# Optimization experiments

Measured on AMD Instinct MI355X. Metric: run time of the kernel, lower is better.

The kernel has to match this reference:

```python
import jax, jax.numpy as jnp
import numpy as np

B, N, D = 16, 2048, 64

def setup_inputs() -> dict:
    key = jax.random.key(0)
    kq, kk, kv = jax.random.split(key, 3)
    q = jax.random.normal(kq, (B, N, D), dtype=jnp.float32)
    k = jax.random.normal(kk, (B, N, D), dtype=jnp.float32)
    v = jax.random.normal(kv, (B, N, D), dtype=jnp.float32)
    scale = jnp.float32(1.0 / np.sqrt(D))  # canonical 1/sqrt(d_head)
    return {"q": q, "k": k, "v": v, "scale": scale}

def reference(q, k, v, scale):
    # attention = softmax((q @ k^T) * scale) over key axis; dropout p=0.0 is identity
    scores = jnp.einsum('bqd,bkd->bqk', q, k) * scale  # [B,N,N]
    attention = jax.nn.softmax(scores, axis=2)
    context = jnp.einsum('bqk,bkd->bqd', attention, v)  # [B,N,D]
    return (context, attention)
```

## Files before the change

### kernel.cpp

```cpp
#include <hip/hip_runtime.h>

#define Bb 16
#define Nn 2048
#define Dd 64

typedef __attribute__((ext_vector_type(8))) short s16x8;
typedef __attribute__((ext_vector_type(4))) float fx4;

__device__ __forceinline__ unsigned short f2bf(float f) {
  union { float f; unsigned u; } v; v.f = f;
  unsigned r = v.u + 0x7FFFu + ((v.u >> 16) & 1u);
  return (unsigned short)(r >> 16);
}

__global__ void k_cvtK(const float* __restrict__ K, unsigned short* __restrict__ Kb) {
  int i = blockIdx.x * 256 + threadIdx.x;
  float4 f = ((const float4*)K)[i];
  ushort4 o;
  o.x = f2bf(f.x); o.y = f2bf(f.y); o.z = f2bf(f.z); o.w = f2bf(f.w);
  ((ushort4*)Kb)[i] = o;
}

__global__ void k_transV(const float* __restrict__ V, unsigned short* __restrict__ VT) {
  __shared__ float tile[32][33];
  int b = blockIdx.z;
  int j0 = blockIdx.x * 32, d0 = blockIdx.y * 32;
  int tx = threadIdx.x, ty = threadIdx.y;
  const float* Vb = V + (size_t)b * Nn * Dd;
  unsigned short* Tb = VT + (size_t)b * Dd * Nn;
  for (int r = ty; r < 32; r += 8)
    tile[r][tx] = Vb[(size_t)(j0 + r) * Dd + d0 + tx];
  __syncthreads();
  for (int r = ty; r < 32; r += 8)
    Tb[(size_t)(d0 + r) * Nn + j0 + tx] = f2bf(tile[tx][r]);
}

__global__ __launch_bounds__(256) void k_attn(
    const float* __restrict__ Q, const unsigned short* __restrict__ Kbf,
    const unsigned short* __restrict__ VTbf, const float* __restrict__ scale_p,
    float* __restrict__ ctx, float* __restrict__ att) {
  const int id = blockIdx.x;
  const int swz = ((id & 7) << 8) | (id >> 3);
  const int b = swz >> 7;
  const int q0 = (swz & 127) << 4;

  const int tid = threadIdx.x;
  const int wave = tid >> 6, lane = tid & 63;
  const int nl = lane & 15, quad = lane >> 4;
  const int qrow = q0 + nl;
  const float c2 = scale_p[0] * 1.44269504088896341f;

  __shared__ float sm[4][16];
  __shared__ float sl[4][16];
  __shared__ __align__(16) float obf[4 * 1024];
  char* pbw = (char*)obf + wave * 4096;

  s16x8 qb[2];
  {
    const float* qp = Q + ((size_t)b * Nn + qrow) * Dd + quad * 8;
#pragma unroll
    for (int kt = 0; kt < 2; ++kt) {
      float4 f0 = *(const float4*)(qp + kt * 32);
      float4 f1 = *(const float4*)(qp + kt * 32 + 4);
      s16x8 t;
      t[0] = (short)f2bf(f0.x); t[1] = (short)f2bf(f0.y);
      t[2] = (short)f2bf(f0.z); t[3] = (short)f2bf(f0.w);
      t[4] = (short)f2bf(f1.x); t[5] = (short)f2bf(f1.y);
      t[6] = (short)f2bf(f1.z); t[7] = (short)f2bf(f1.w);
      qb[kt] = t;
    }
  }
  const unsigned short* Kb = Kbf + (size_t)b * Nn * Dd;
  const unsigned short* VTb = VTbf + (size_t)b * Dd * Nn;
  float* attb = att + (size_t)b * Nn * Nn;

  float m = -3.0e38f, l = 0.0f;

  for (int t = 0; t < 4; ++t) {
    const int k0 = (wave * 4 + t) * 128;
    fx4 s[8];
#pragma unroll
    for (int nt = 0; nt < 8; ++nt) s[nt] = (fx4){0.f, 0.f, 0.f, 0.f};
#pragma unroll
    for (int nt = 0; nt < 8; ++nt) {
      const s16x8* ka =
          (const s16x8*)(Kb + ((size_t)(k0 + nt * 16 + nl)) * Dd + quad * 8);
      s[nt] = __builtin_amdgcn_mfma_f32_16x16x32_bf16(ka[0], qb[0], s[nt], 0, 0, 0);
      s[nt] = __builtin_amdgcn_mfma_f32_16x16x32_bf16(ka[4], qb[1], s[nt], 0, 0, 0);
    }
    float x0 = s[0][0], x1 = s[0][1], x2 = s[0][2], x3 = s[0][3];
#pragma unroll
    for (int nt = 1; nt < 8; ++nt) {
      x0 = fmaxf(x0, s[nt][0]); x1 = fmaxf(x1, s[nt][1]);
      x2 = fmaxf(x2, s[nt][2]); x3 = fmaxf(x3, s[nt][3]);
    }
    float lm = fmaxf(fmaxf(x0, x1), fmaxf(x2, x3));
    float mn = fmaxf(m, lm * c2);
    float a0 = 0.f, a1 = 0.f, a2 = 0.f, a3 = 0.f;
#pragma unroll
    for (int nt = 0; nt < 8; ++nt) {
      a0 += exp2f(fmaf(s[nt][0], c2, -mn));
      a1 += exp2f(fmaf(s[nt][1], c2, -mn));
      a2 += exp2f(fmaf(s[nt][2], c2, -mn));
      a3 += exp2f(fmaf(s[nt][3], c2, -mn));
    }
    float ls = (a0 + a1) + (a2 + a3);
    l = l * exp2f(m - mn) + ls;
    m = mn;
  }
#pragma unroll
  for (int mask = 16; mask <= 32; mask <<= 1) {
    float om = __shfl_xor(m, mask, 64);
    float ol = __shfl_xor(l, mask, 64);
    float mn = fmaxf(m, om);
    l = l * exp2f(m - mn) + ol * exp2f(om - mn);
    m = mn;
  }
  if (lane < 16) { sm[wave][lane] = m; sl[wave][lane] = l; }
  __syncthreads();
  float rinv;
  {
    float M = sm[0][nl], L = sl[0][nl];
#pragma unroll
    for (int j = 1; j < 4; ++j) {
      float mj = sm[j][nl], lj = sl[j][nl];
      float mn = fmaxf(M, mj);
      L = L * exp2f(M - mn) + lj * exp2f(mj - mn);
      M = mn;
    }
    m = M;
    rinv = 1.0f / L;
  }

  fx4 o[4];
#pragma unroll
  for (int d = 0; d < 4; ++d) o[d] = (fx4){0.f, 0.f, 0.f, 0.f};

  for (int t = 0; t < 4; ++t) {
    const int k0 = (wave * 4 + t) * 128;
    fx4 s[8];
#pragma unroll
    for (int nt = 0; nt < 8; ++nt) s[nt] = (fx4){0.f, 0.f, 0.f, 0.f};
#pragma unroll
    for (int nt = 0; nt < 8; ++nt) {
      const s16x8* ka =
          (const s16x8*)(Kb + ((size_t)(k0 + nt * 16 + nl)) * Dd + quad * 8);
      s[nt] = __builtin_amdgcn_mfma_f32_16x16x32_bf16(ka[0], qb[0], s[nt], 0, 0, 0);
      s[nt] = __builtin_amdgcn_mfma_f32_16x16x32_bf16(ka[4], qb[1], s[nt], 0, 0, 0);
    }
#pragma unroll
    for (int nt = 0; nt < 8; ++nt) {
#pragma unroll
      for (int r = 0; r < 4; ++r)
        s[nt][r] = exp2f(fmaf(s[nt][r], c2, -m)) * rinv;
      unsigned long long pk =
          (unsigned long long)f2bf(s[nt][0]) |
          ((unsigned long long)f2bf(s[nt][1]) << 16) |
          ((unsigned long long)f2bf(s[nt][2]) << 32) |
          ((unsigned long long)f2bf(s[nt][3]) << 48);
      *(unsigned long long*)(pbw + nl * 256 +
                             ((nt * 32 + quad * 8) ^ ((nl & 7) << 4))) = pk;
    }
#pragma unroll
    for (int kt = 0; kt < 4; ++kt) {
      s16x8 pa = *(const s16x8*)(pbw + nl * 256 +
                                 ((kt * 64 + quad * 16) ^ ((nl & 7) << 4)));
#pragma unroll
      for (int ntd = 0; ntd < 4; ++ntd) {
        s16x8 vb = *(const s16x8*)(VTb + ((size_t)(ntd * 16 + nl)) * Nn + k0 +
                                   kt * 32 + quad * 8);
        o[ntd] = __builtin_amdgcn_mfma_f32_16x16x32_bf16(pa, vb, o[ntd], 0, 0, 0);
      }
    }
    __builtin_amdgcn_sched_barrier(0);
#pragma unroll
    for (int nt = 0; nt < 8; ++nt)
      __builtin_nontemporal_store(
          s[nt], (fx4*)(attb + (size_t)qrow * Nn + k0 + nt * 16 + quad * 4));
  }

  {
    float* myob = obf + wave * 1024;
#pragma unroll
    for (int ntd = 0; ntd < 4; ++ntd)
#pragma unroll
      for (int r = 0; r < 4; ++r) {
        const int row = quad * 4 + r;
        const int unit = ntd * 4 + (nl >> 2);
        const int su = unit ^ (row & 7);
        myob[row * 64 + su * 4 + (nl & 3)] = o[ntd][r];
      }
  }
  __syncthreads();
  {
    const int row = tid >> 4;
    const int un = tid & 15;
    const int su = un ^ (row & 7);
    fx4 a = *(const fx4*)&obf[row * 64 + su * 4];
#pragma unroll
    for (int j = 1; j < 4; ++j) {
      fx4 tt = *(const fx4*)&obf[j * 1024 + row * 64 + su * 4];
      a[0] += tt[0]; a[1] += tt[1]; a[2] += tt[2]; a[3] += tt[3];
    }
    *(fx4*)(ctx + ((size_t)b * Nn + q0 + row) * Dd + un * 4) = a;
  }
}

extern "C" void kernel_launch(void* const* d_in, const int* in_sizes, int n_in,
                              void* d_out, int out_size, void* d_ws, size_t ws_size,
                              hipStream_t stream) {
  const float* q = (const float*)d_in[0];
  const float* k = (const float*)d_in[1];
  const float* v = (const float*)d_in[2];
  const float* scale = (const float*)d_in[3];

  float* ctx = (float*)d_out;
  float* att = ctx + (size_t)Bb * Nn * Dd;

  unsigned short* Kbf = (unsigned short*)d_ws;
  unsigned short* VTbf = Kbf + (size_t)Bb * Nn * Dd;

  hipLaunchKernelGGL(k_cvtK, dim3((Bb * Nn * Dd) / (256 * 4)), dim3(256), 0, stream,
                     k, Kbf);
  hipLaunchKernelGGL(k_transV, dim3(Nn / 32, Dd / 32, Bb), dim3(32, 8), 0, stream,
                     v, VTbf);
  hipLaunchKernelGGL(k_attn, dim3(Bb * Nn / 16), dim3(256), 0, stream,
                     q, Kbf, VTbf, scale, ctx, att);
}
```

Before: 444.1 us.

## Software-pipeline K and V register prefetch in second attention pass

The second pass now uses 64-key tiles and keeps the K and V^T fragments for the next tile in registers. The prefetch loads are issued right after the QK MFMAs and PV MFMAs of the current tile, so global load latency overlaps with the exp/bf16 packing and the attention-matrix stores. The per-wave LDS staging for P shrinks to match the smaller tile, and a __syncthreads is added before the output buffer is reused. In exchange, register pressure rises, and the last iteration wraps around and issues redundant prefetch loads.

```diff
diff --git a/kernel.cpp b/kernel.cpp
--- a/kernel.cpp
+++ b/kernel.cpp
@@ -54,6 +54,7 @@
   __shared__ float sl[4][16];
   __shared__ __align__(16) float obf[4 * 1024];
   char* pbw = (char*)obf + wave * 4096;
+  const int swz8 = (nl & 7) << 4;
 
   s16x8 qb[2];
   {
@@ -136,20 +137,41 @@
 #pragma unroll
   for (int d = 0; d < 4; ++d) o[d] = (fx4){0.f, 0.f, 0.f, 0.f};
 
-  for (int t = 0; t < 4; ++t) {
-    const int k0 = (wave * 4 + t) * 128;
-    fx4 s[8];
-#pragma unroll
-    for (int nt = 0; nt < 8; ++nt) s[nt] = (fx4){0.f, 0.f, 0.f, 0.f};
-#pragma unroll
-    for (int nt = 0; nt < 8; ++nt) {
+  s16x8 kr[8], vr[8];
+  {
+    const int k0 = wave * 512;
+#pragma unroll
+    for (int nt = 0; nt < 4; ++nt) {
       const s16x8* ka =
           (const s16x8*)(Kb + ((size_t)(k0 + nt * 16 + nl)) * Dd + quad * 8);
-      s[nt] = __builtin_amdgcn_mfma_f32_16x16x32_bf16(ka[0], qb[0], s[nt], 0, 0, 0);
-      s[nt] = __builtin_amdgcn_mfma_f32_16x16x32_bf16(ka[4], qb[1], s[nt], 0, 0, 0);
-    }
-#pragma unroll
-    for (int nt = 0; nt < 8; ++nt) {
+      kr[2 * nt] = ka[0]; kr[2 * nt + 1] = ka[4];
+    }
+#pragma unroll
+    for (int kt = 0; kt < 2; ++kt)
+#pragma unroll
+      for (int ntd = 0; ntd < 4; ++ntd)
+        vr[kt * 4 + ntd] = *(const s16x8*)(VTb + ((size_t)(ntd * 16 + nl)) * Nn +
+                                           k0 + kt * 32 + quad * 8);
+  }
+
+  for (int t = 0; t < 8; ++t) {
+    const int k0 = wave * 512 + t * 64;
+    const int k0n = wave * 512 + ((t + 1) & 7) * 64;
+    fx4 s[4];
+#pragma unroll
+    for (int nt = 0; nt < 4; ++nt) {
+      s[nt] = (fx4){0.f, 0.f, 0.f, 0.f};
+      s[nt] = __builtin_amdgcn_mfma_f32_16x16x32_bf16(kr[2 * nt], qb[0], s[nt], 0, 0, 0);
+      s[nt] = __builtin_amdgcn_mfma_f32_16x16x32_bf16(kr[2 * nt + 1], qb[1], s[nt], 0, 0, 0);
+    }
+#pragma unroll
+    for (int nt = 0; nt < 4; ++nt) {
+      const s16x8* ka =
+          (const s16x8*)(Kb + ((size_t)(k0n + nt * 16 + nl)) * Dd + quad * 8);
+      kr[2 * nt] = ka[0]; kr[2 * nt + 1] = ka[4];
+    }
+#pragma unroll
+    for (int nt = 0; nt < 4; ++nt) {
 #pragma unroll
       for (int r = 0; r < 4; ++r)
         s[nt][r] = exp2f(fmaf(s[nt][r], c2, -m)) * rinv;
@@ -158,27 +180,32 @@
           ((unsigned long long)f2bf(s[nt][1]) << 16) |
           ((unsigned long long)f2bf(s[nt][2]) << 32) |
           ((unsigned long long)f2bf(s[nt][3]) << 48);
-      *(unsigned long long*)(pbw + nl * 256 +
-                             ((nt * 32 + quad * 8) ^ ((nl & 7) << 4))) = pk;
-    }
-#pragma unroll
-    for (int kt = 0; kt < 4; ++kt) {
-      s16x8 pa = *(const s16x8*)(pbw + nl * 256 +
-                                 ((kt * 64 + quad * 16) ^ ((nl & 7) << 4)));
-#pragma unroll
-      for (int ntd = 0; ntd < 4; ++ntd) {
-        s16x8 vb = *(const s16x8*)(VTb + ((size_t)(ntd * 16 + nl)) * Nn + k0 +
-                                   kt * 32 + quad * 8);
-        o[ntd] = __builtin_amdgcn_mfma_f32_16x16x32_bf16(pa, vb, o[ntd], 0, 0, 0);
-      }
-    }
+      *(unsigned long long*)(pbw + nl * 128 + ((nt * 32 + quad * 8) ^ swz8)) = pk;
+    }
+#pragma unroll
+    for (int kt = 0; kt < 2; ++kt) {
+      s16x8 pa =
+          *(const s16x8*)(pbw + nl * 128 + ((kt * 64 + quad * 16) ^ swz8));
+#pragma unroll
+      for (int ntd = 0; ntd < 4; ++ntd)
+        o[ntd] = __builtin_amdgcn_mfma_f32_16x16x32_bf16(pa, vr[kt * 4 + ntd],
+                                                         o[ntd], 0, 0, 0);
+    }
+#pragma unroll
+    for (int kt = 0; kt < 2; ++kt)
+#pragma unroll
+      for (int ntd = 0; ntd < 4; ++ntd)
+        vr[kt * 4 + ntd] = *(const s16x8*)(VTb + ((size_t)(ntd * 16 + nl)) * Nn +
+                                           k0n + kt * 32 + quad * 8);
     __builtin_amdgcn_sched_barrier(0);
 #pragma unroll
-    for (int nt = 0; nt < 8; ++nt)
+    for (int nt = 0; nt < 4; ++nt)
       __builtin_nontemporal_store(
           s[nt], (fx4*)(attb + (size_t)qrow * Nn + k0 + nt * 16 + quad * 4));
-  }
-
+    __builtin_amdgcn_sched_barrier(0);
+  }
+
+  __syncthreads();
   {
     float* myob = obf + wave * 1024;
 #pragma unroll
```

New measurement: 455.2 us. 1.02x slower.
